# Optimization experiments

Measured on AMD Instinct MI355X. Metric: run time of the kernel, lower is better.

Reference implementation:

```python
import jax, jax.numpy as jnp
import numpy as np

N_WIRES = 8
DIM = 1 << N_WIRES  # 256
ENC_WIRES = [0, 1, 2, 2, 4, 5, 6, 7]  # faithful to source: wire 2 twice, wire 3 skipped

# Precompute composed CNOT-ring permutation: CNOT(0,1),(1,2),...,(6,7),(7,0)
_idx = np.arange(DIM)
_perm = _idx.copy()
for c, t in [(k, k + 1) for k in range(N_WIRES - 1)] + [(N_WIRES - 1, 0)]:
    cbit = (_idx >> (N_WIRES - 1 - c)) & 1
    P = np.where(cbit == 1, _idx ^ (1 << (N_WIRES - 1 - t)), _idx)
    _perm = _perm[P]
CNOT_PERM = jnp.asarray(_perm)
# Pauli-Z sign table per wire: (8, 256)
Z_SIGNS = jnp.asarray(1 - 2 * ((_idx[None, :] >> (N_WIRES - 1 - np.arange(N_WIRES)[:, None])) & 1)).astype(jnp.float32)


def _rx(state, wire, theta):
    """Apply RX(theta) on `wire`. state: (N, 256) complex64, theta: (N,) float."""
    N = state.shape[0]
    s = state.reshape(N, 1 << wire, 2, 1 << (N_WIRES - 1 - wire))
    half = theta * 0.5
    c = jnp.cos(half)[:, None, None]
    sn = jnp.sin(half)[:, None, None]
    a, b = s[:, :, 0, :], s[:, :, 1, :]
    top = c * a - 1j * sn * b
    bot = -1j * sn * a + c * b
    return jnp.stack([top, bot], axis=2).reshape(N, DIM)


def qlayer(tokens, theta):
    """Batched 8-qubit circuit: encoder RX(x_k), trainable RX(theta_w), CNOT ring, <Z_w>.
    tokens: (N, 8) float32 -> (N, 8) float32 expectation values."""
    N = tokens.shape[0]
    state = jnp.zeros((N, DIM), jnp.complex64).at[:, 0].set(1.0)
    for k, w in enumerate(ENC_WIRES):
        state = _rx(state, w, tokens[:, k])
    for w in range(N_WIRES):
        state = _rx(state, w, jnp.broadcast_to(theta[w], (N,)))
    state = state[:, CNOT_PERM]
    probs = state.real ** 2 + state.imag ** 2  # (N, 256)
    return probs @ Z_SIGNS.T  # (N, 8)


def setup_inputs() -> dict:
    key = jax.random.key(0)
    kx, kt = jax.random.split(key)
    x = jax.random.normal(kx, (16, 1024, 8), dtype=jnp.float32)
    theta = jax.random.uniform(kt, (8,), dtype=jnp.float32, minval=0.0, maxval=2.0 * np.pi)
    return {"x": x, "theta": theta}


def reference(x, theta):
    B, S, E = x.shape
    H, dk = 2, E // 2
    tok = x.reshape(B * S, E)
    # Original computes Q, K, V with the SAME shared q_layer on the SAME input,
    # so Q == K == V; compute once.
    qkv = qlayer(tok, theta).reshape(B, S, E)
    h = qkv.reshape(B, S, H, dk).transpose(0, 2, 1, 3)  # (B,H,S,dk)
    scores = jnp.einsum('bhqd,bhkd->bhqk', h, h) / np.sqrt(dk).astype(np.float32)
    w = jax.nn.softmax(scores, axis=-1)  # (eval mode: dropout inactive)
    attn = jnp.einsum('bhqk,bhkd->bhqd', w, h)
    concat = attn.transpose(0, 2, 1, 3).reshape(B, S, E)
    out = qlayer(concat.reshape(B * S, E), theta).reshape(B, S, E)
    return out
```

## Files before the change

### kernel.cpp

```cpp
#include <hip/hip_runtime.h>

#define SEQ 1024

typedef __attribute__((ext_vector_type(2))) float f2;

static __device__ __forceinline__ int lds_addr(int k) {
    return (k << 3) + ((k >> 7) << 2);
}

static __device__ __forceinline__ void qrow(const float th[8], const float y[8], float o[8]) {
    float a[8];
    a[0] = y[0] + th[0];
    a[1] = y[1] + th[1];
    a[2] = y[2] + y[3] + th[2];
    a[3] = th[3];
    a[4] = y[4] + th[4];
    a[5] = y[5] + th[5];
    a[6] = y[6] + th[6];
    a[7] = y[7] + th[7];
    float c[8];
#pragma unroll
    for (int w = 0; w < 8; ++w) c[w] = __cosf(a[w]);
    o[1] = c[0] * c[1];
#pragma unroll
    for (int w = 2; w < 8; ++w) o[w] = o[w - 1] * c[w];
    float s = c[7];
#pragma unroll
    for (int w = 6; w >= 1; --w) s *= c[w];
    o[0] = s;
}

__global__ __launch_bounds__(256, 4) void mhaq_fused(const float* __restrict__ x,
                                                     const float* __restrict__ theta,
                                                     float* __restrict__ out) {
    __shared__ __align__(16) float h_lds[8 * SEQ + 7 * 4 + 4];

    const int b   = blockIdx.x >> 6;
    const int qof = (blockIdx.x & 63) << 4;
    const int t   = threadIdx.x;

    float th[8];
#pragma unroll
    for (int w = 0; w < 8; ++w) th[w] = theta[w];

    const float4* xb = (const float4*)(x + (size_t)b * SEQ * 8);
    float4 v0[4], v1[4];
#pragma unroll
    for (int r = 0; r < 4; ++r) {
        const int k = t + (r << 8);
        v0[r] = xb[2 * k];
        v1[r] = xb[2 * k + 1];
    }
#pragma unroll
    for (int r = 0; r < 4; ++r) {
        const int k = t + (r << 8);
        const float y[8] = {v0[r].x, v0[r].y, v0[r].z, v0[r].w,
                            v1[r].x, v1[r].y, v1[r].z, v1[r].w};
        float o[8];
        qrow(th, y, o);
        float4* p = (float4*)&h_lds[lds_addr(k)];
        p[0] = make_float4(o[0], o[1], o[2], o[3]);
        p[1] = make_float4(o[4], o[5], o[6], o[7]);
    }
    __syncthreads();

    const int lane  = t & 63;
    const int wv    = t >> 6;
    const int qiw   = lane >> 4;
    const int chunk = lane & 15;
    const int q     = qof + (wv << 2) + qiw;

    const float qscale = 0.5f * 1.44269504f;
    f2 qv01, qv23, qv45, qv67;
    {
        const float* qp = &h_lds[lds_addr(q)];
        qv01 = f2{qp[0], qp[1]} * qscale;
        qv23 = f2{qp[2], qp[3]} * qscale;
        qv45 = f2{qp[4], qp[5]} * qscale;
        qv67 = f2{qp[6], qp[7]} * qscale;
    }

    float l0 = 0.f, l1 = 0.f;
    f2 a01 = {0.f, 0.f}, a23 = {0.f, 0.f}, a45 = {0.f, 0.f}, a67 = {0.f, 0.f};

    int base = lds_addr(chunk << 6);
#pragma unroll 4
    for (int i = 0; i < 64; ++i) {
        const float4 k0 = *(const float4*)&h_lds[base];
        const float4 k1 = *(const float4*)&h_lds[base + 4];
        base += 8;
        const f2 k01 = {k0.x, k0.y}, k23 = {k0.z, k0.w};
        const f2 k45 = {k1.x, k1.y}, k67 = {k1.z, k1.w};
        const f2 d0 = qv01 * k01 + qv23 * k23;
        const f2 d1 = qv45 * k45 + qv67 * k67;
        const float e0 = __builtin_amdgcn_exp2f(d0.x + d0.y);
        const float e1 = __builtin_amdgcn_exp2f(d1.x + d1.y);
        l0 += e0;
        l1 += e1;
        const f2 e0v = {e0, e0}, e1v = {e1, e1};
        a01 += e0v * k01;
        a23 += e0v * k23;
        a45 += e1v * k45;
        a67 += e1v * k67;
    }

    float red[10] = {l0, l1, a01.x, a01.y, a23.x, a23.y, a45.x, a45.y, a67.x, a67.y};
#pragma unroll
    for (int m = 1; m < 16; m <<= 1) {
#pragma unroll
        for (int j = 0; j < 10; ++j) red[j] += __shfl_xor(red[j], m);
    }

    if (chunk == 0) {
        const float inv0 = 1.0f / red[0];
        const float inv1 = 1.0f / red[1];
        float y[8];
#pragma unroll
        for (int d = 0; d < 4; ++d) {
            y[d]     = red[2 + d] * inv0;
            y[4 + d] = red[6 + d] * inv1;
        }
        float o[8];
        qrow(th, y, o);
        float4* op = (float4*)(out + ((size_t)(b * SEQ + q)) * 8);
        op[0] = make_float4(o[0], o[1], o[2], o[3]);
        op[1] = make_float4(o[4], o[5], o[6], o[7]);
    }
}

extern "C" void kernel_launch(void* const* d_in, const int* in_sizes, int n_in,
                              void* d_out, int out_size, void* d_ws, size_t ws_size,
                              hipStream_t stream) {
    const float* x     = (const float*)d_in[0];
    const float* theta = (const float*)d_in[1];
    float* out         = (float*)d_out;
    mhaq_fused<<<dim3(16 * 64), dim3(256), 0, stream>>>(x, theta, out);
}
```

Measured before the change: 66.84 us.

## Process four queries per lane to reuse each key load across queries

Each lane now holds four queries and scans 16 keys, instead of one query per 16-lane group scanning 64 keys. Every key vector read from LDS is therefore reused across four queries, cutting LDS traffic per exponential by a factor of four. The LDS padding changes to one pad every 16 rows so the new strided per-lane key access avoids bank conflicts. In exchange the cross-lane reduction grows to 40 values over 6 shuffle stages, and register pressure rises, which could limit occupancy under the launch bounds.

```diff
diff --git a/kernel.cpp b/kernel.cpp
--- a/kernel.cpp
+++ b/kernel.cpp
@@ -5,7 +5,7 @@
 typedef __attribute__((ext_vector_type(2))) float f2;
 
 static __device__ __forceinline__ int lds_addr(int k) {
-    return (k << 3) + ((k >> 7) << 2);
+    return (k << 3) + ((k >> 4) << 2);
 }
 
 static __device__ __forceinline__ void qrow(const float th[8], const float y[8], float o[8]) {
@@ -33,7 +33,7 @@
 __global__ __launch_bounds__(256, 4) void mhaq_fused(const float* __restrict__ x,
                                                      const float* __restrict__ theta,
                                                      float* __restrict__ out) {
-    __shared__ __align__(16) float h_lds[8 * SEQ + 7 * 4 + 4];
+    __shared__ __align__(16) float h_lds[8448];
 
     const int b   = blockIdx.x >> 6;
     const int qof = (blockIdx.x & 63) << 4;
@@ -66,63 +66,93 @@
 
     const int lane  = t & 63;
     const int wv    = t >> 6;
-    const int qiw   = lane >> 4;
-    const int chunk = lane & 15;
-    const int q     = qof + (wv << 2) + qiw;
+    const int qbase = qof + (wv << 2);
 
     const float qscale = 0.5f * 1.44269504f;
-    f2 qv01, qv23, qv45, qv67;
-    {
-        const float* qp = &h_lds[lds_addr(q)];
-        qv01 = f2{qp[0], qp[1]} * qscale;
-        qv23 = f2{qp[2], qp[3]} * qscale;
-        qv45 = f2{qp[4], qp[5]} * qscale;
-        qv67 = f2{qp[6], qp[7]} * qscale;
+    f2 qv[4][4];
+#pragma unroll
+    for (int qq = 0; qq < 4; ++qq) {
+        const float* qp = &h_lds[lds_addr(qbase + qq)];
+        qv[qq][0] = f2{qp[0], qp[1]} * qscale;
+        qv[qq][1] = f2{qp[2], qp[3]} * qscale;
+        qv[qq][2] = f2{qp[4], qp[5]} * qscale;
+        qv[qq][3] = f2{qp[6], qp[7]} * qscale;
     }
 
-    float l0 = 0.f, l1 = 0.f;
-    f2 a01 = {0.f, 0.f}, a23 = {0.f, 0.f}, a45 = {0.f, 0.f}, a67 = {0.f, 0.f};
+    float l0[4] = {0.f, 0.f, 0.f, 0.f};
+    float l1[4] = {0.f, 0.f, 0.f, 0.f};
+    f2 a01[4], a23[4], a45[4], a67[4];
+#pragma unroll
+    for (int qq = 0; qq < 4; ++qq) {
+        a01[qq] = f2{0.f, 0.f};
+        a23[qq] = f2{0.f, 0.f};
+        a45[qq] = f2{0.f, 0.f};
+        a67[qq] = f2{0.f, 0.f};
+    }
 
-    int base = lds_addr(chunk << 6);
+    int base = lds_addr(lane << 4);
 #pragma unroll 4
-    for (int i = 0; i < 64; ++i) {
+    for (int i = 0; i < 16; ++i) {
         const float4 k0 = *(const float4*)&h_lds[base];
         const float4 k1 = *(const float4*)&h_lds[base + 4];
         base += 8;
         const f2 k01 = {k0.x, k0.y}, k23 = {k0.z, k0.w};
         const f2 k45 = {k1.x, k1.y}, k67 = {k1.z, k1.w};
-        const f2 d0 = qv01 * k01 + qv23 * k23;
-        const f2 d1 = qv45 * k45 + qv67 * k67;
-        const float e0 = __builtin_amdgcn_exp2f(d0.x + d0.y);
-        const float e1 = __builtin_amdgcn_exp2f(d1.x + d1.y);
-        l0 += e0;
-        l1 += e1;
-        const f2 e0v = {e0, e0}, e1v = {e1, e1};
-        a01 += e0v * k01;
-        a23 += e0v * k23;
-        a45 += e1v * k45;
-        a67 += e1v * k67;
+#pragma unroll
+        for (int qq = 0; qq < 4; ++qq) {
+            const f2 d0 = qv[qq][0] * k01 + qv[qq][1] * k23;
+            const f2 d1 = qv[qq][2] * k45 + qv[qq][3] * k67;
+            const float e0 = __builtin_amdgcn_exp2f(d0.x + d0.y);
+            const float e1 = __builtin_amdgcn_exp2f(d1.x + d1.y);
+            l0[qq] += e0;
+            l1[qq] += e1;
+            const f2 e0v = {e0, e0}, e1v = {e1, e1};
+            a01[qq] += e0v * k01;
+            a23[qq] += e0v * k23;
+            a45[qq] += e1v * k45;
+            a67[qq] += e1v * k67;
+        }
     }
 
-    float red[10] = {l0, l1, a01.x, a01.y, a23.x, a23.y, a45.x, a45.y, a67.x, a67.y};
+    float red[40];
 #pragma unroll
-    for (int m = 1; m < 16; m <<= 1) {
+    for (int qq = 0; qq < 4; ++qq) {
+        red[qq * 10 + 0] = l0[qq];
+        red[qq * 10 + 1] = l1[qq];
+        red[qq * 10 + 2] = a01[qq].x;
+        red[qq * 10 + 3] = a01[qq].y;
+        red[qq * 10 + 4] = a23[qq].x;
+        red[qq * 10 + 5] = a23[qq].y;
+        red[qq * 10 + 6] = a45[qq].x;
+        red[qq * 10 + 7] = a45[qq].y;
+        red[qq * 10 + 8] = a67[qq].x;
+        red[qq * 10 + 9] = a67[qq].y;
+    }
 #pragma unroll
-        for (int j = 0; j < 10; ++j) red[j] += __shfl_xor(red[j], m);
+    for (int m = 1; m < 64; m <<= 1) {
+#pragma unroll
+        for (int j = 0; j < 40; ++j) red[j] += __shfl_xor(red[j], m);
     }
 
-    if (chunk == 0) {
-        const float inv0 = 1.0f / red[0];
-        const float inv1 = 1.0f / red[1];
+    float sel[10];
+#pragma unroll
+    for (int j = 0; j < 10; ++j) {
+        const float v01 = (lane & 1) ? red[10 + j] : red[j];
+        const float v23 = (lane & 1) ? red[30 + j] : red[20 + j];
+        sel[j] = (lane & 2) ? v23 : v01;
+    }
+    if (lane < 4) {
+        const float inv0 = 1.0f / sel[0];
+        const float inv1 = 1.0f / sel[1];
         float y[8];
 #pragma unroll
         for (int d = 0; d < 4; ++d) {
-            y[d]     = red[2 + d] * inv0;
-            y[4 + d] = red[6 + d] * inv1;
+            y[d]     = sel[2 + d] * inv0;
+            y[4 + d] = sel[6 + d] * inv1;
         }
         float o[8];
         qrow(th, y, o);
-        float4* op = (float4*)(out + ((size_t)(b * SEQ + q)) * 8);
+        float4* op = (float4*)(out + ((size_t)(b * SEQ + qbase + lane)) * 8);
         op[0] = make_float4(o[0], o[1], o[2], o[3]);
         op[1] = make_float4(o[4], o[5], o[6], o[7]);
     }
```

Result: slower. 69.92 us (+4.6%).
